# Optimization experiments

Hardware: AMD Instinct MI355X
Metric: run time of the kernel (lower is better)

## Reference

```python
import jax, jax.numpy as jnp
import numpy as np

LATENT = 512
RNN = 512
CODE = 512
INP = 2
MIX = 5
BATCH = 4096
SEGMENTS = 512


def _p(key, shape, scale=0.05):
    return jax.random.normal(key, shape, dtype=jnp.float32) * scale


def setup_inputs() -> dict:
    key = jax.random.key(0)
    ks = jax.random.split(key, 20)
    return {
        "latent": jax.random.normal(ks[0], (BATCH, LATENT), dtype=jnp.float32),
        "W_unpack": _p(ks[1], (CODE, LATENT)),
        "b_unpack": _p(ks[2], (CODE,)),
        "W_ih1": _p(ks[3], (4 * RNN, CODE + INP)),
        "W_hh1": _p(ks[4], (4 * RNN, RNN)),
        "b_ih1": _p(ks[5], (4 * RNN,)),
        "b_hh1": _p(ks[6], (4 * RNN,)),
        "W_ih2": _p(ks[7], (4 * RNN, RNN)),
        "W_hh2": _p(ks[8], (4 * RNN, RNN)),
        "b_ih2": _p(ks[9], (4 * RNN,)),
        "b_hh2": _p(ks[10], (4 * RNN,)),
        "W_mu": _p(ks[11], (MIX, RNN)),
        "b_mu": _p(ks[12], (MIX,)),
        "W_var": _p(ks[13], (MIX, RNN)),
        "b_var": _p(ks[14], (MIX,)),
        "W_mix": _p(ks[15], (MIX, RNN)),
        "b_mix": _p(ks[16], (MIX,)),
        "eps": jax.random.normal(ks[17], (SEGMENTS, BATCH, 1), dtype=jnp.float32),
        "num_segments": SEGMENTS,
    }


def _lstm_cell(x, h, c, W_ih, W_hh, b_ih, b_hh):
    # PyTorch LSTMCell: gate order i, f, g, o
    gates = x @ W_ih.T + b_ih + h @ W_hh.T + b_hh
    i, f, g, o = jnp.split(gates, 4, axis=-1)
    c_new = jax.nn.sigmoid(f) * c + jax.nn.sigmoid(i) * jnp.tanh(g)
    h_new = jax.nn.sigmoid(o) * jnp.tanh(c_new)
    return h_new, c_new


def reference(latent, W_unpack, b_unpack, W_ih1, W_hh1, b_ih1, b_hh1,
              W_ih2, W_hh2, b_ih2, b_hh2, W_mu, b_mu, W_var, b_var,
              W_mix, b_mix, eps, num_segments):
    t = 0.0  # default temperature arg
    B = latent.shape[0]
    idea = jnp.tanh(latent @ W_unpack.T + b_unpack)  # [B, CODE]

    def step(carry, eps_s):
        prev, h1, c1, h2, c2 = carry
        x = jnp.concatenate([idea, prev], axis=-1)          # [B, CODE+2]
        h1, c1 = _lstm_cell(x, h1, c1, W_ih1, W_hh1, b_ih1, b_hh1)
        h2, c2 = _lstm_cell(h1, h2, c2, W_ih2, W_hh2, b_ih2, b_hh2)
        rho = jax.nn.softmax(h2 @ W_mix.T + b_mix, axis=-1)  # [B, MIX]
        mu = jnp.sum(rho * (h2 @ W_mu.T + b_mu), axis=-1, keepdims=True)
        sigma = jnp.sum(rho * jnp.exp(h2 @ W_var.T + b_var - t), axis=-1, keepdims=True)
        angles = jnp.tanh(mu + sigma * eps_s)                # rsample + tanh, [B, 1]
        prev = jnp.concatenate([angles, jnp.zeros_like(angles)], axis=-1)
        return (prev, h1, c1, h2, c2), angles

    z = jnp.zeros((B, RNN), dtype=latent.dtype)
    carry0 = (jnp.zeros((B, INP), dtype=latent.dtype), z, z, z, z)
    _, angles = jax.lax.scan(step, carry0, eps)              # [S, B, 1]
    level = jnp.concatenate([angles, jnp.zeros_like(angles)], axis=-1)  # [S, B, 2]
    return jnp.transpose(level, (1, 0, 2))                   # [B, S, 2]
```

## Files before the change

kernel.cpp:

```cpp
#include <hip/hip_runtime.h>
#include <stdint.h>

#define BATCH 4096
#define RNN   512
#define SEGS  512

typedef __attribute__((ext_vector_type(8))) short bf16x8;
typedef __attribute__((ext_vector_type(4))) float f32x4;

#define MODE_TANH  0
#define MODE_BASE  1
#define MODE_CELL1 2
#define MODE_CELL2 3

__device__ __forceinline__ unsigned short f2bf(float f){
  unsigned u = __float_as_uint(f);
  u += 0x7FFF + ((u >> 16) & 1);
  return (unsigned short)(u >> 16);
}
__device__ __forceinline__ float bf2f(unsigned short s){
  return __uint_as_float(((unsigned)s) << 16);
}
__device__ __forceinline__ float fsigmoid(float x){ return 1.0f / (1.0f + __expf(-x)); }
__device__ __forceinline__ float ftanh(float x){
  float e = __expf(-2.0f * fabsf(x));
  float t = (1.0f - e) / (1.0f + e);
  return copysignf(t, x);
}


__global__ void prep_cvt(const float* __restrict__ x, short* __restrict__ y, int n){
  int i = blockIdx.x * 256 + threadIdx.x;
  if (i < n) y[i] = (short)f2bf(x[i]);
}

__global__ void prep_reorder(
    const float* __restrict__ W_ih1, const float* __restrict__ W_hh1,
    const float* __restrict__ b_ih1, const float* __restrict__ b_hh1,
    const float* __restrict__ W_ih2, const float* __restrict__ W_hh2,
    const float* __restrict__ b_ih2, const float* __restrict__ b_hh2,
    short* __restrict__ Wr1, short* __restrict__ W1c,
    short* __restrict__ Wr2i, short* __restrict__ Wr2h,
    float* __restrict__ w1r, float* __restrict__ b1r, float* __restrict__ b2r)
{
  int idx = blockIdx.x * 256 + threadIdx.x;
  if (idx >= 2048 * 512) return;
  int rn = idx >> 9;
  int k  = idx & 511;
  int j = rn >> 2, g = rn & 3;
  int ro = g * 512 + j;
  Wr1 [idx] = (short)f2bf(W_hh1[(size_t)ro * 512 + k]);
  W1c [idx] = (short)f2bf(W_ih1[(size_t)ro * 514 + k]);
  Wr2i[idx] = (short)f2bf(W_ih2[(size_t)ro * 512 + k]);
  Wr2h[idx] = (short)f2bf(W_hh2[(size_t)ro * 512 + k]);
  if (k == 0){
    w1r[rn] = W_ih1[(size_t)ro * 514 + 512];
    b1r[rn] = b_ih1[ro] + b_hh1[ro];
    b2r[rn] = b_ih2[ro] + b_hh2[ro];
  }
}

__global__ __launch_bounds__(256) void gemm_fused(
    const short* __restrict__ A1, const short* __restrict__ B1,
    const short* __restrict__ A2, const short* __restrict__ B2,
    int k1, int k2, int N, int mode,
    const float* __restrict__ bias,
    const float* __restrict__ base1,
    const float* __restrict__ w1r,
    const float* __restrict__ ang,
    float* __restrict__ cbuf,
    void* __restrict__ outp)
{
  __shared__ __align__(16) short As[128 * 72];
  __shared__ __align__(16) short Bs[128 * 72];
  const int tid  = threadIdx.x;
  const int lane = tid & 63;
  const int wave = tid >> 6;
  const int wm = wave >> 1, wn = wave & 1;
  const int m0 = blockIdx.y * 128, n0 = blockIdx.x * 128;

  f32x4 acc[4][4];
  #pragma unroll
  for (int i = 0; i < 4; i++)
    #pragma unroll
    for (int j = 0; j < 4; j++)
      acc[i][j] = (f32x4){0.f, 0.f, 0.f, 0.f};

  const int nk = (k1 + k2) >> 6;
  for (int it = 0; it < nk; ++it){
    int ko = it << 6;
    const short* Ap; const short* Bp; int kk;
    if (ko < k1){ Ap = A1; Bp = B1; kk = ko; }
    else        { Ap = A2; Bp = B2; kk = ko - k1; }
    #pragma unroll
    for (int i = 0; i < 4; i++){
      int c = i * 256 + tid;
      int row = c >> 3, c8 = (c & 7) << 3;
      *(uint4*)&As[row * 72 + c8] = *(const uint4*)&Ap[(size_t)(m0 + row) * 512 + kk + c8];
      *(uint4*)&Bs[row * 72 + c8] = *(const uint4*)&Bp[(size_t)(n0 + row) * 512 + kk + c8];
    }
    __syncthreads();
    #pragma unroll
    for (int kw = 0; kw < 2; ++kw){
      bf16x8 af[4], bfr[4];
      const int ro = (lane & 15) * 72 + kw * 32 + (lane >> 4) * 8;
      #pragma unroll
      for (int f = 0; f < 4; f++){
        af[f]  = *(const bf16x8*)&As[(wm * 64 + f * 16) * 72 + ro];
        bfr[f] = *(const bf16x8*)&Bs[(wn * 64 + f * 16) * 72 + ro];
      }
      #pragma unroll
      for (int mf = 0; mf < 4; mf++)
        #pragma unroll
        for (int nf = 0; nf < 4; nf++)
          acc[mf][nf] = __builtin_amdgcn_mfma_f32_16x16x32_bf16(af[mf], bfr[nf], acc[mf][nf], 0, 0, 0);
    }
    __syncthreads();
  }

  const int lr = (lane >> 4) * 4;
  const int lc = lane & 15;

  if (mode == MODE_TANH){
    unsigned short* out = (unsigned short*)outp;
    #pragma unroll
    for (int mf = 0; mf < 4; mf++)
      #pragma unroll
      for (int nf = 0; nf < 4; nf++)
        #pragma unroll
        for (int r = 0; r < 4; r++){
          int grow = m0 + wm * 64 + mf * 16 + lr + r;
          int gcol = n0 + wn * 64 + nf * 16 + lc;
          float v = acc[mf][nf][r] + bias[gcol];
          out[(size_t)grow * N + gcol] = f2bf(ftanh(v));
        }
  } else if (mode == MODE_BASE){
    float* out = (float*)outp;
    #pragma unroll
    for (int mf = 0; mf < 4; mf++)
      #pragma unroll
      for (int nf = 0; nf < 4; nf++)
        #pragma unroll
        for (int r = 0; r < 4; r++){
          int grow = m0 + wm * 64 + mf * 16 + lr + r;
          int gcol = n0 + wn * 64 + nf * 16 + lc;
          out[(size_t)grow * N + gcol] = acc[mf][nf][r] + bias[gcol];
        }
  } else {
    unsigned short* hout = (unsigned short*)outp;
    const int q = lane & 3;
    #pragma unroll
    for (int mf = 0; mf < 4; mf++)
      #pragma unroll
      for (int nf = 0; nf < 4; nf++)
        #pragma unroll
        for (int r = 0; r < 4; r++){
          int grow = m0 + wm * 64 + mf * 16 + lr + r;
          int gcol = n0 + wn * 64 + nf * 16 + lc;
          float v = acc[mf][nf][r];
          if (mode == MODE_CELL1)
            v += base1[(size_t)grow * 2048 + gcol] + ang[grow] * w1r[gcol];
          else
            v += bias[gcol];
          float x1 = __shfl_xor(v, 1);
          float x2 = __shfl_xor(v, 2);
          float x3 = __shfl_xor(v, 3);
          if (q == 0){
            int j = gcol >> 2;
            size_t ci = (size_t)grow * 512 + j;
            float co = cbuf[ci];
            float cn = fsigmoid(x1) * co + fsigmoid(v) * ftanh(x2);
            float hn = fsigmoid(x3) * ftanh(cn);
            cbuf[ci] = cn;
            hout[ci] = f2bf(hn);
          }
        }
  }
}

__global__ __launch_bounds__(256) void head_step(
    const short* __restrict__ h2,
    const float* __restrict__ Wmu,  const float* __restrict__ bmu,
    const float* __restrict__ Wvar, const float* __restrict__ bvar,
    const float* __restrict__ Wmix, const float* __restrict__ bmix,
    const float* __restrict__ eps,  float* __restrict__ ang,
    float* __restrict__ out, int s)
{
  const int lane = threadIdx.x & 63;
  const int wave = threadIdx.x >> 6;
  const int row = blockIdx.x * 4 + wave;

  uint4 hv = *(const uint4*)&h2[(size_t)row * 512 + lane * 8];
  const unsigned short* hs = (const unsigned short*)&hv;
  float h[8];
  #pragma unroll
  for (int j = 0; j < 8; j++) h[j] = bf2f(hs[j]);

  float p[15];
  #pragma unroll
  for (int k = 0; k < 5; k++){
    const float4* wm4 = (const float4*)(Wmu  + (size_t)k * 512 + lane * 8);
    const float4* wv4 = (const float4*)(Wvar + (size_t)k * 512 + lane * 8);
    const float4* wx4 = (const float4*)(Wmix + (size_t)k * 512 + lane * 8);
    float4 a0 = wm4[0], a1 = wm4[1];
    float4 v0 = wv4[0], v1 = wv4[1];
    float4 x0 = wx4[0], x1 = wx4[1];
    p[k]      = h[0]*a0.x + h[1]*a0.y + h[2]*a0.z + h[3]*a0.w + h[4]*a1.x + h[5]*a1.y + h[6]*a1.z + h[7]*a1.w;
    p[5 + k]  = h[0]*v0.x + h[1]*v0.y + h[2]*v0.z + h[3]*v0.w + h[4]*v1.x + h[5]*v1.y + h[6]*v1.z + h[7]*v1.w;
    p[10 + k] = h[0]*x0.x + h[1]*x0.y + h[2]*x0.z + h[3]*x0.w + h[4]*x1.x + h[5]*x1.y + h[6]*x1.z + h[7]*x1.w;
  }
  #pragma unroll
  for (int k = 0; k < 15; k++){
    #pragma unroll
    for (int off = 1; off < 64; off <<= 1)
      p[k] += __shfl_xor(p[k], off);
  }
  if (lane == 0){
    float l[5], mx = -1e30f;
    #pragma unroll
    for (int k = 0; k < 5; k++){ l[k] = p[10 + k] + bmix[k]; mx = fmaxf(mx, l[k]); }
    float se = 0.f, e[5];
    #pragma unroll
    for (int k = 0; k < 5; k++){ e[k] = __expf(l[k] - mx); se += e[k]; }
    float inv = 1.0f / se, mu = 0.f, sg = 0.f;
    #pragma unroll
    for (int k = 0; k < 5; k++){
      float rho = e[k] * inv;
      mu += rho * (p[k] + bmu[k]);
      sg += rho * __expf(p[5 + k] + bvar[k]);
    }
    float a = ftanh(mu + sg * eps[(size_t)s * BATCH + row]);
    ang[row] = a;
    size_t o = ((size_t)row * SEGS + s) * 2;
    out[o]     = a;
    out[o + 1] = 0.0f;
  }
}


extern "C" void kernel_launch(void* const* d_in, const int* in_sizes, int n_in,
                              void* d_out, int out_size, void* d_ws, size_t ws_size,
                              hipStream_t stream)
{
  const float* latent   = (const float*)d_in[0];
  const float* W_unpack = (const float*)d_in[1];
  const float* b_unpack = (const float*)d_in[2];
  const float* W_ih1    = (const float*)d_in[3];
  const float* W_hh1    = (const float*)d_in[4];
  const float* b_ih1    = (const float*)d_in[5];
  const float* b_hh1    = (const float*)d_in[6];
  const float* W_ih2    = (const float*)d_in[7];
  const float* W_hh2    = (const float*)d_in[8];
  const float* b_ih2    = (const float*)d_in[9];
  const float* b_hh2    = (const float*)d_in[10];
  const float* W_mu     = (const float*)d_in[11];
  const float* b_mu     = (const float*)d_in[12];
  const float* W_var    = (const float*)d_in[13];
  const float* b_var    = (const float*)d_in[14];
  const float* W_mix    = (const float*)d_in[15];
  const float* b_mix    = (const float*)d_in[16];
  const float* eps      = (const float*)d_in[17];
  float* out = (float*)d_out;

  char* p = (char*)d_ws;
  auto alloc = [&](size_t b) -> void* {
    void* r = (void*)p;
    p += (b + 255) & ~(size_t)255;
    return r;
  };
  short* latb  = (short*)alloc((size_t)BATCH * 512 * 2);
  short* Wub   = (short*)alloc((size_t)512 * 512 * 2);
  short* idea  = (short*)alloc((size_t)BATCH * 512 * 2);
  float* base1 = (float*)alloc((size_t)BATCH * 2048 * 4);
  short* Wr1   = (short*)alloc((size_t)2048 * 512 * 2);
  short* W1c   = (short*)alloc((size_t)2048 * 512 * 2);
  short* Wr2i  = (short*)alloc((size_t)2048 * 512 * 2);
  short* Wr2h  = (short*)alloc((size_t)2048 * 512 * 2);
  float* w1r   = (float*)alloc(2048 * 4);
  float* b1r   = (float*)alloc(2048 * 4);
  float* b2r   = (float*)alloc(2048 * 4);
  short* h1a   = (short*)alloc((size_t)BATCH * 512 * 2);
  short* h1b   = (short*)alloc((size_t)BATCH * 512 * 2);
  short* h2a   = (short*)alloc((size_t)BATCH * 512 * 2);
  short* h2b   = (short*)alloc((size_t)BATCH * 512 * 2);
  float* c1    = (float*)alloc((size_t)BATCH * 512 * 4);
  float* c2    = (float*)alloc((size_t)BATCH * 512 * 4);
  float* ang   = (float*)alloc(BATCH * 4);
  short* h1[2] = {h1a, h1b};
  short* h2[2] = {h2a, h2b};

  hipMemsetAsync(h1[0], 0, (size_t)BATCH * 512 * 2, stream);
  hipMemsetAsync(h2[0], 0, (size_t)BATCH * 512 * 2, stream);
  hipMemsetAsync(c1, 0, (size_t)BATCH * 512 * 4, stream);
  hipMemsetAsync(c2, 0, (size_t)BATCH * 512 * 4, stream);
  hipMemsetAsync(ang, 0, BATCH * 4, stream);

  prep_cvt<<<(BATCH * 512) / 256, 256, 0, stream>>>(latent, latb, BATCH * 512);
  prep_cvt<<<(512 * 512) / 256, 256, 0, stream>>>(W_unpack, Wub, 512 * 512);
  prep_reorder<<<(2048 * 512) / 256, 256, 0, stream>>>(
      W_ih1, W_hh1, b_ih1, b_hh1, W_ih2, W_hh2, b_ih2, b_hh2,
      Wr1, W1c, Wr2i, Wr2h, w1r, b1r, b2r);

  dim3 blk(256);
  gemm_fused<<<dim3(512 / 128, 32), blk, 0, stream>>>(
      latb, Wub, nullptr, nullptr, 512, 0, 512, MODE_TANH,
      b_unpack, nullptr, nullptr, nullptr, nullptr, (void*)idea);
  gemm_fused<<<dim3(2048 / 128, 32), blk, 0, stream>>>(
      idea, W1c, nullptr, nullptr, 512, 0, 2048, MODE_BASE,
      b1r, nullptr, nullptr, nullptr, nullptr, (void*)base1);

  int cur = 0;
  for (int s = 0; s < SEGS; ++s){
    gemm_fused<<<dim3(16, 32), blk, 0, stream>>>(
        h1[cur], Wr1, nullptr, nullptr, 512, 0, 2048, MODE_CELL1,
        nullptr, base1, w1r, ang, c1, (void*)h1[cur ^ 1]);
    gemm_fused<<<dim3(16, 32), blk, 0, stream>>>(
        h1[cur ^ 1], Wr2i, h2[cur], Wr2h, 512, 512, 2048, MODE_CELL2,
        b2r, nullptr, nullptr, nullptr, c2, (void*)h2[cur ^ 1]);
    head_step<<<BATCH / 4, 256, 0, stream>>>(
        h2[cur ^ 1], W_mu, b_mu, W_var, b_var, W_mix, b_mix, eps, ang, out, s);
    cur ^= 1;
  }
}
```

Baseline: 63.81 ms.

## Replace per-step kernel launches with a persistent RNN kernel using group barriers

Replaces the 1536 per-step launches (two LSTM GEMMs plus head) with one persistent kernel of 256 blocks. Each block owns a 128x256 tile, and blocks covering the same 128 rows synchronise through atomic counters in global memory. The rewrite also loads tiles with direct global-to-LDS loads in a swizzled layout, stores base1 in bf16 with a row-interleaved layout, and folds the mixture head into the kernel with bf16 weights. This removes launch overhead and inter-kernel gaps, but relies on all 256 blocks being co-resident to avoid deadlock and adds spin-wait costs.

Measured after the change: 202.8 ms. +217.8%, slower.

```diff
diff --git a/kernel.cpp b/kernel.cpp
--- a/kernel.cpp
+++ b/kernel.cpp
@@ -2,16 +2,14 @@
 #include <stdint.h>
 
 #define BATCH 4096
-#define RNN   512
 #define SEGS  512
 
 typedef __attribute__((ext_vector_type(8))) short bf16x8;
 typedef __attribute__((ext_vector_type(4))) float f32x4;
 
-#define MODE_TANH  0
-#define MODE_BASE  1
-#define MODE_CELL1 2
-#define MODE_CELL2 3
+#define GLD_LDS16(g, l) \
+  __builtin_amdgcn_global_load_lds((const __attribute__((address_space(1))) void*)(g), \
+                                   (__attribute__((address_space(3))) void*)(l), 16, 0, 0)
 
 __device__ __forceinline__ unsigned short f2bf(float f){
   unsigned u = __float_as_uint(f);
@@ -60,25 +58,38 @@
   }
 }
 
-__global__ __launch_bounds__(256) void gemm_fused(
-    const short* __restrict__ A1, const short* __restrict__ B1,
-    const short* __restrict__ A2, const short* __restrict__ B2,
-    int k1, int k2, int N, int mode,
-    const float* __restrict__ bias,
-    const float* __restrict__ base1,
-    const float* __restrict__ w1r,
-    const float* __restrict__ ang,
-    float* __restrict__ cbuf,
-    void* __restrict__ outp)
+__global__ void prep_whead(const float* __restrict__ Wmu, const float* __restrict__ Wvar,
+                           const float* __restrict__ Wmix, short* __restrict__ Wh){
+  int i = blockIdx.x * 256 + threadIdx.x;
+  if (i >= 15 * 512) return;
+  int n = i >> 9, k = i & 511;
+  float v = (n < 5) ? Wmu[n * 512 + k] : (n < 10) ? Wvar[(n - 5) * 512 + k]
+          : Wmix[(n - 10) * 512 + k];
+  Wh[i] = (short)f2bf(v);
+}
+
+__global__ __launch_bounds__(256) void gemm_pre(
+    const short* A, const short* B,
+    int N, int mode, const float* bias,
+    unsigned short* outp)
 {
-  __shared__ __align__(16) short As[128 * 72];
-  __shared__ __align__(16) short Bs[128 * 72];
-  const int tid  = threadIdx.x;
-  const int lane = tid & 63;
-  const int wave = tid >> 6;
+  __shared__ __align__(16) short As[8192];
+  __shared__ __align__(16) short Bs[8192];
+  const int tid = threadIdx.x, lane = tid & 63, wave = tid >> 6;
   const int wm = wave >> 1, wn = wave & 1;
   const int m0 = blockIdx.y * 128, n0 = blockIdx.x * 128;
 
+  int aoff[4], boff[4];
+  #pragma unroll
+  for (int j = 0; j < 4; j++){
+    int c = (wave * 4 + j) * 64 + lane;
+    int quad = c & 3, r16 = (c >> 2) & 15, kw = (c >> 6) & 1, g = c >> 7;
+    int row = g * 16 + r16, col = kw * 32 + quad * 8;
+    aoff[j] = (m0 + row) * 512 + col;
+    boff[j] = (n0 + row) * 512 + col;
+  }
+  const int fro = ((lane & 15) * 4 + (lane >> 4)) * 8;
+
   f32x4 acc[4][4];
   #pragma unroll
   for (int i = 0; i < 4; i++)
@@ -86,28 +97,21 @@
     for (int j = 0; j < 4; j++)
       acc[i][j] = (f32x4){0.f, 0.f, 0.f, 0.f};
 
-  const int nk = (k1 + k2) >> 6;
-  for (int it = 0; it < nk; ++it){
-    int ko = it << 6;
-    const short* Ap; const short* Bp; int kk;
-    if (ko < k1){ Ap = A1; Bp = B1; kk = ko; }
-    else        { Ap = A2; Bp = B2; kk = ko - k1; }
-    #pragma unroll
-    for (int i = 0; i < 4; i++){
-      int c = i * 256 + tid;
-      int row = c >> 3, c8 = (c & 7) << 3;
-      *(uint4*)&As[row * 72 + c8] = *(const uint4*)&Ap[(size_t)(m0 + row) * 512 + kk + c8];
-      *(uint4*)&Bs[row * 72 + c8] = *(const uint4*)&Bp[(size_t)(n0 + row) * 512 + kk + c8];
+  for (int it = 0; it < 8; ++it){
+    const int kk = it << 6;
+    #pragma unroll
+    for (int j = 0; j < 4; ++j){
+      GLD_LDS16(A + aoff[j] + kk, (char*)As + (wave * 4 + j) * 1024);
+      GLD_LDS16(B + boff[j] + kk, (char*)Bs + (wave * 4 + j) * 1024);
     }
     __syncthreads();
     #pragma unroll
     for (int kw = 0; kw < 2; ++kw){
       bf16x8 af[4], bfr[4];
-      const int ro = (lane & 15) * 72 + kw * 32 + (lane >> 4) * 8;
       #pragma unroll
       for (int f = 0; f < 4; f++){
-        af[f]  = *(const bf16x8*)&As[(wm * 64 + f * 16) * 72 + ro];
-        bfr[f] = *(const bf16x8*)&Bs[(wn * 64 + f * 16) * 72 + ro];
+        af[f]  = *(const bf16x8*)&As[((wm * 4 + f) * 2 + kw) * 512 + fro];
+        bfr[f] = *(const bf16x8*)&Bs[((wn * 4 + f) * 2 + kw) * 512 + fro];
       }
       #pragma unroll
       for (int mf = 0; mf < 4; mf++)
@@ -120,120 +124,260 @@
 
   const int lr = (lane >> 4) * 4;
   const int lc = lane & 15;
-
-  if (mode == MODE_TANH){
-    unsigned short* out = (unsigned short*)outp;
-    #pragma unroll
-    for (int mf = 0; mf < 4; mf++)
-      #pragma unroll
-      for (int nf = 0; nf < 4; nf++)
-        #pragma unroll
-        for (int r = 0; r < 4; r++){
-          int grow = m0 + wm * 64 + mf * 16 + lr + r;
-          int gcol = n0 + wn * 64 + nf * 16 + lc;
-          float v = acc[mf][nf][r] + bias[gcol];
-          out[(size_t)grow * N + gcol] = f2bf(ftanh(v));
-        }
-  } else if (mode == MODE_BASE){
-    float* out = (float*)outp;
-    #pragma unroll
-    for (int mf = 0; mf < 4; mf++)
-      #pragma unroll
-      for (int nf = 0; nf < 4; nf++)
-        #pragma unroll
-        for (int r = 0; r < 4; r++){
-          int grow = m0 + wm * 64 + mf * 16 + lr + r;
-          int gcol = n0 + wn * 64 + nf * 16 + lc;
-          out[(size_t)grow * N + gcol] = acc[mf][nf][r] + bias[gcol];
-        }
-  } else {
-    unsigned short* hout = (unsigned short*)outp;
-    const int q = lane & 3;
-    #pragma unroll
-    for (int mf = 0; mf < 4; mf++)
-      #pragma unroll
-      for (int nf = 0; nf < 4; nf++)
-        #pragma unroll
-        for (int r = 0; r < 4; r++){
-          int grow = m0 + wm * 64 + mf * 16 + lr + r;
-          int gcol = n0 + wn * 64 + nf * 16 + lc;
-          float v = acc[mf][nf][r];
-          if (mode == MODE_CELL1)
-            v += base1[(size_t)grow * 2048 + gcol] + ang[grow] * w1r[gcol];
-          else
-            v += bias[gcol];
-          float x1 = __shfl_xor(v, 1);
-          float x2 = __shfl_xor(v, 2);
-          float x3 = __shfl_xor(v, 3);
-          if (q == 0){
-            int j = gcol >> 2;
-            size_t ci = (size_t)grow * 512 + j;
-            float co = cbuf[ci];
-            float cn = fsigmoid(x1) * co + fsigmoid(v) * ftanh(x2);
-            float hn = fsigmoid(x3) * ftanh(cn);
-            cbuf[ci] = cn;
-            hout[ci] = f2bf(hn);
+  #pragma unroll
+  for (int mf = 0; mf < 4; mf++)
+    #pragma unroll
+    for (int nf = 0; nf < 4; nf++)
+      #pragma unroll
+      for (int r = 0; r < 4; r++){
+        int grow = m0 + wm * 64 + mf * 16 + lr + r;
+        int gcol = n0 + wn * 64 + nf * 16 + lc;
+        float v = acc[mf][nf][r] + bias[gcol];
+        if (mode == 0)
+          outp[(size_t)grow * N + gcol] = f2bf(ftanh(v));
+        else
+          outp[((size_t)(grow >> 2) * 2048 + gcol) * 4 + (grow & 3)] = f2bf(v);
+      }
+}
+
+
+__device__ __forceinline__ void run_tile256(
+    const short* A1, const short* B1, const short* A2, const short* B2,
+    int nk1, int nk2, const int* aoff, const int* boff,
+    short* As, short* Bs, int wave, int wm, int wn, int fro,
+    f32x4 (&acc)[4][8])
+{
+  #pragma unroll
+  for (int i = 0; i < 4; i++)
+    #pragma unroll
+    for (int j = 0; j < 8; j++)
+      acc[i][j] = (f32x4){0.f, 0.f, 0.f, 0.f};
+
+  const int nk = nk1 + nk2;
+  for (int it = 0; it < nk; ++it){
+    const short* Ap = (it < nk1) ? A1 : A2;
+    const short* Bp = (it < nk1) ? B1 : B2;
+    const int kk = ((it < nk1) ? it : it - nk1) << 6;
+    #pragma unroll
+    for (int j = 0; j < 4; ++j)
+      GLD_LDS16(Ap + aoff[j] + kk, (char*)As + (wave * 4 + j) * 1024);
+    #pragma unroll
+    for (int j = 0; j < 8; ++j)
+      GLD_LDS16(Bp + boff[j] + kk, (char*)Bs + (wave * 8 + j) * 1024);
+    __syncthreads();
+    #pragma unroll
+    for (int kw = 0; kw < 2; ++kw){
+      bf16x8 af[4], bfr[8];
+      #pragma unroll
+      for (int f = 0; f < 4; f++)
+        af[f]  = *(const bf16x8*)&As[((wm * 4 + f) * 2 + kw) * 512 + fro];
+      #pragma unroll
+      for (int f = 0; f < 8; f++)
+        bfr[f] = *(const bf16x8*)&Bs[((wn * 8 + f) * 2 + kw) * 512 + fro];
+      #pragma unroll
+      for (int mf = 0; mf < 4; mf++)
+        #pragma unroll
+        for (int nf = 0; nf < 8; nf++)
+          acc[mf][nf] = __builtin_amdgcn_mfma_f32_16x16x32_bf16(af[mf], bfr[nf], acc[mf][nf], 0, 0, 0);
+    }
+    __syncthreads();
+  }
+}
+
+__device__ __forceinline__ void mgroup_bar(int* cnt, int target, int tid){
+  __syncthreads();
+  if (tid == 0){
+    __threadfence();
+    __hip_atomic_fetch_add(cnt, 1, __ATOMIC_RELEASE, __HIP_MEMORY_SCOPE_AGENT);
+    while (__hip_atomic_load(cnt, __ATOMIC_ACQUIRE, __HIP_MEMORY_SCOPE_AGENT) < target)
+      __builtin_amdgcn_s_sleep(1);
+    __threadfence();
+  }
+  __syncthreads();
+}
+
+__global__ __launch_bounds__(256, 1) void persistent_rnn(
+    short* h1A, short* h1B, short* h2A, short* h2B,
+    const short* Wr1, const short* Wr2i, const short* Wr2h,
+    const unsigned short* base1,
+    const float* w1r, const float* b2r,
+    const short* Whead,
+    const float* bmu, const float* bvar,
+    const float* bmix, const float* eps,
+    float* angG, float* c1G, float* c2G,
+    int* barA, int* barB, int* flagH,
+    float* out)
+{
+  __shared__ __align__(16) short As[8192];
+  __shared__ __align__(16) short Bs[16384];
+  __shared__ float headP[16 * 16];
+  __shared__ float angSf[128];
+
+  const int tid = threadIdx.x, lane = tid & 63, wave = tid >> 6;
+  const int wm = wave >> 1, wn = wave & 1;
+  const int bid = blockIdx.x;
+  const int m_idx = bid >> 3, n_idx = bid & 7;
+  const int m0 = m_idx * 128, n0 = n_idx * 256;
+
+  int aoff[4], boff[8];
+  #pragma unroll
+  for (int j = 0; j < 4; j++){
+    int c = (wave * 4 + j) * 64 + lane;
+    int quad = c & 3, r16 = (c >> 2) & 15, kw = (c >> 6) & 1, g = c >> 7;
+    aoff[j] = (m0 + g * 16 + r16) * 512 + kw * 32 + quad * 8;
+  }
+  #pragma unroll
+  for (int j = 0; j < 8; j++){
+    int c = (wave * 8 + j) * 64 + lane;
+    int quad = c & 3, r16 = (c >> 2) & 15, kw = (c >> 6) & 1, g = c >> 7;
+    boff[j] = (n0 + g * 16 + r16) * 512 + kw * 32 + quad * 8;
+  }
+  const int fro = ((lane & 15) * 4 + (lane >> 4)) * 8;
+  const int lr = (lane >> 4) * 4;
+  const int lc = lane & 15;
+  const int q = lane & 3;
+
+  if (tid < 128) angSf[tid] = 0.f;
+  __syncthreads();
+
+  f32x4 acc[4][8];
+  short* h1buf[2] = {h1A, h1B};
+  short* h2buf[2] = {h2A, h2B};
+  int cur = 0;
+
+  #pragma clang loop unroll(disable)
+  for (int s = 0; s < SEGS; ++s){
+    const short* h1c = h1buf[cur];
+    short*       h1n = h1buf[cur ^ 1];
+    const short* h2c = h2buf[cur];
+    short*       h2n = h2buf[cur ^ 1];
+
+    run_tile256(h1c, Wr1, nullptr, nullptr, 8, 0, aoff, boff,
+                As, Bs, wave, wm, wn, fro, acc);
+
+    if (s > 0){
+      if (tid == 0){
+        while (__hip_atomic_load(&flagH[m_idx], __ATOMIC_ACQUIRE, __HIP_MEMORY_SCOPE_AGENT) < 8 * s)
+          __builtin_amdgcn_s_sleep(1);
+        __threadfence();
+      }
+      __syncthreads();
+      if (tid < 128)
+        angSf[tid] = __hip_atomic_load(&angG[m0 + tid], __ATOMIC_RELAXED, __HIP_MEMORY_SCOPE_AGENT);
+      __syncthreads();
+    }
+
+    {
+      unsigned short* hout = (unsigned short*)h1n;
+      #pragma unroll
+      for (int mf = 0; mf < 4; mf++)
+        #pragma unroll
+        for (int nf = 0; nf < 8; nf++){
+          const int growb = m0 + wm * 64 + mf * 16 + lr;
+          const int gcol  = n0 + wn * 128 + nf * 16 + lc;
+          const float wv = w1r[gcol];
+          ushort4 b4 = *(const ushort4*)&base1[((size_t)(growb >> 2) * 2048 + gcol) * 4];
+          const unsigned short bb4[4] = {b4.x, b4.y, b4.z, b4.w};
+          #pragma unroll
+          for (int r = 0; r < 4; r++){
+            int grow = growb + r;
+            float v = acc[mf][nf][r] + bf2f(bb4[r]) + angSf[grow - m0] * wv;
+            float x1 = __shfl_xor(v, 1);
+            float x2 = __shfl_xor(v, 2);
+            float x3 = __shfl_xor(v, 3);
+            if (q == 0){
+              size_t ci = (size_t)grow * 512 + (gcol >> 2);
+              float co = c1G[ci];
+              float cn = fsigmoid(x1) * co + fsigmoid(v) * ftanh(x2);
+              float hn = fsigmoid(x3) * ftanh(cn);
+              c1G[ci] = cn;
+              hout[ci] = f2bf(hn);
+            }
           }
         }
-  }
-}
-
-__global__ __launch_bounds__(256) void head_step(
-    const short* __restrict__ h2,
-    const float* __restrict__ Wmu,  const float* __restrict__ bmu,
-    const float* __restrict__ Wvar, const float* __restrict__ bvar,
-    const float* __restrict__ Wmix, const float* __restrict__ bmix,
-    const float* __restrict__ eps,  float* __restrict__ ang,
-    float* __restrict__ out, int s)
-{
-  const int lane = threadIdx.x & 63;
-  const int wave = threadIdx.x >> 6;
-  const int row = blockIdx.x * 4 + wave;
-
-  uint4 hv = *(const uint4*)&h2[(size_t)row * 512 + lane * 8];
-  const unsigned short* hs = (const unsigned short*)&hv;
-  float h[8];
-  #pragma unroll
-  for (int j = 0; j < 8; j++) h[j] = bf2f(hs[j]);
-
-  float p[15];
-  #pragma unroll
-  for (int k = 0; k < 5; k++){
-    const float4* wm4 = (const float4*)(Wmu  + (size_t)k * 512 + lane * 8);
-    const float4* wv4 = (const float4*)(Wvar + (size_t)k * 512 + lane * 8);
-    const float4* wx4 = (const float4*)(Wmix + (size_t)k * 512 + lane * 8);
-    float4 a0 = wm4[0], a1 = wm4[1];
-    float4 v0 = wv4[0], v1 = wv4[1];
-    float4 x0 = wx4[0], x1 = wx4[1];
-    p[k]      = h[0]*a0.x + h[1]*a0.y + h[2]*a0.z + h[3]*a0.w + h[4]*a1.x + h[5]*a1.y + h[6]*a1.z + h[7]*a1.w;
-    p[5 + k]  = h[0]*v0.x + h[1]*v0.y + h[2]*v0.z + h[3]*v0.w + h[4]*v1.x + h[5]*v1.y + h[6]*v1.z + h[7]*v1.w;
-    p[10 + k] = h[0]*x0.x + h[1]*x0.y + h[2]*x0.z + h[3]*x0.w + h[4]*x1.x + h[5]*x1.y + h[6]*x1.z + h[7]*x1.w;
-  }
-  #pragma unroll
-  for (int k = 0; k < 15; k++){
-    #pragma unroll
-    for (int off = 1; off < 64; off <<= 1)
-      p[k] += __shfl_xor(p[k], off);
-  }
-  if (lane == 0){
-    float l[5], mx = -1e30f;
-    #pragma unroll
-    for (int k = 0; k < 5; k++){ l[k] = p[10 + k] + bmix[k]; mx = fmaxf(mx, l[k]); }
-    float se = 0.f, e[5];
-    #pragma unroll
-    for (int k = 0; k < 5; k++){ e[k] = __expf(l[k] - mx); se += e[k]; }
-    float inv = 1.0f / se, mu = 0.f, sg = 0.f;
-    #pragma unroll
-    for (int k = 0; k < 5; k++){
-      float rho = e[k] * inv;
-      mu += rho * (p[k] + bmu[k]);
-      sg += rho * __expf(p[5 + k] + bvar[k]);
-    }
-    float a = ftanh(mu + sg * eps[(size_t)s * BATCH + row]);
-    ang[row] = a;
-    size_t o = ((size_t)row * SEGS + s) * 2;
-    out[o]     = a;
-    out[o + 1] = 0.0f;
+    }
+    mgroup_bar(&barA[m_idx], 8 * (s + 1), tid);
+
+    run_tile256(h1n, Wr2i, h2c, Wr2h, 8, 8, aoff, boff,
+                As, Bs, wave, wm, wn, fro, acc);
+    {
+      unsigned short* hout = (unsigned short*)h2n;
+      #pragma unroll
+      for (int mf = 0; mf < 4; mf++)
+        #pragma unroll
+        for (int nf = 0; nf < 8; nf++){
+          const int growb = m0 + wm * 64 + mf * 16 + lr;
+          const int gcol  = n0 + wn * 128 + nf * 16 + lc;
+          const float bv = b2r[gcol];
+          #pragma unroll
+          for (int r = 0; r < 4; r++){
+            int grow = growb + r;
+            float v = acc[mf][nf][r] + bv;
+            float x1 = __shfl_xor(v, 1);
+            float x2 = __shfl_xor(v, 2);
+            float x3 = __shfl_xor(v, 3);
+            if (q == 0){
+              size_t ci = (size_t)grow * 512 + (gcol >> 2);
+              float co = c2G[ci];
+              float cn = fsigmoid(x1) * co + fsigmoid(v) * ftanh(x2);
+              float hn = fsigmoid(x3) * ftanh(cn);
+              c2G[ci] = cn;
+              hout[ci] = f2bf(hn);
+            }
+          }
+        }
+    }
+    mgroup_bar(&barB[m_idx], 8 * (s + 1), tid);
+
+    {
+      const int rr = tid & 15, o = tid >> 4;
+      const int row = m0 + n_idx * 16 + rr;
+      if (o < 15){
+        float pv = 0.f;
+        const unsigned short* hp = (const unsigned short*)h2n + (size_t)row * 512;
+        const unsigned short* wp = (const unsigned short*)Whead + o * 512;
+        for (int k = 0; k < 64; k++){
+          uint4 hv = *(const uint4*)(hp + k * 8);
+          uint4 wv = *(const uint4*)(wp + k * 8);
+          const unsigned short* hh = (const unsigned short*)&hv;
+          const unsigned short* ww = (const unsigned short*)&wv;
+          #pragma unroll
+          for (int e = 0; e < 8; e++)
+            pv += bf2f(hh[e]) * bf2f(ww[e]);
+        }
+        headP[rr * 16 + o] = pv;
+      }
+      __syncthreads();
+      if (tid < 16){
+        float pp[15];
+        #pragma unroll
+        for (int k = 0; k < 15; k++) pp[k] = headP[tid * 16 + k];
+        float l[5], mx = -1e30f;
+        #pragma unroll
+        for (int k = 0; k < 5; k++){ l[k] = pp[10 + k] + bmix[k]; mx = fmaxf(mx, l[k]); }
+        float se = 0.f, e5[5];
+        #pragma unroll
+        for (int k = 0; k < 5; k++){ e5[k] = __expf(l[k] - mx); se += e5[k]; }
+        float inv = 1.0f / se, mu = 0.f, sg = 0.f;
+        #pragma unroll
+        for (int k = 0; k < 5; k++){
+          float rho = e5[k] * inv;
+          mu += rho * (pp[k] + bmu[k]);
+          sg += rho * __expf(pp[5 + k] + bvar[k]);
+        }
+        const int row2 = m0 + n_idx * 16 + tid;
+        float a = ftanh(mu + sg * eps[(size_t)s * BATCH + row2]);
+        __hip_atomic_store(&angG[row2], a, __ATOMIC_RELAXED, __HIP_MEMORY_SCOPE_AGENT);
+        size_t oo = ((size_t)row2 * SEGS + s) * 2;
+        out[oo] = a; out[oo + 1] = 0.0f;
+      }
+      __syncthreads();
+      if (tid == 0){
+        __threadfence();
+        __hip_atomic_fetch_add(&flagH[m_idx], 1, __ATOMIC_RELEASE, __HIP_MEMORY_SCOPE_AGENT);
+      }
+    }
+    cur ^= 1;
   }
 }
 
@@ -271,11 +415,12 @@
   short* latb  = (short*)alloc((size_t)BATCH * 512 * 2);
   short* Wub   = (short*)alloc((size_t)512 * 512 * 2);
   short* idea  = (short*)alloc((size_t)BATCH * 512 * 2);
-  float* base1 = (float*)alloc((size_t)BATCH * 2048 * 4);
+  unsigned short* base1 = (unsigned short*)alloc((size_t)BATCH * 2048 * 2);
   short* Wr1   = (short*)alloc((size_t)2048 * 512 * 2);
   short* W1c   = (short*)alloc((size_t)2048 * 512 * 2);
   short* Wr2i  = (short*)alloc((size_t)2048 * 512 * 2);
   short* Wr2h  = (short*)alloc((size_t)2048 * 512 * 2);
+  short* Whead = (short*)alloc((size_t)15 * 512 * 2);
   float* w1r   = (float*)alloc(2048 * 4);
   float* b1r   = (float*)alloc(2048 * 4);
   float* b2r   = (float*)alloc(2048 * 4);
@@ -286,39 +431,30 @@
   float* c1    = (float*)alloc((size_t)BATCH * 512 * 4);
   float* c2    = (float*)alloc((size_t)BATCH * 512 * 4);
   float* ang   = (float*)alloc(BATCH * 4);
-  short* h1[2] = {h1a, h1b};
-  short* h2[2] = {h2a, h2b};
-
-  hipMemsetAsync(h1[0], 0, (size_t)BATCH * 512 * 2, stream);
-  hipMemsetAsync(h2[0], 0, (size_t)BATCH * 512 * 2, stream);
-  hipMemsetAsync(c1, 0, (size_t)BATCH * 512 * 4, stream);
-  hipMemsetAsync(c2, 0, (size_t)BATCH * 512 * 4, stream);
-  hipMemsetAsync(ang, 0, BATCH * 4, stream);
+  int*   barA  = (int*)alloc(32 * 4);
+  int*   barB  = (int*)alloc(32 * 4);
+  int*   flagH = (int*)alloc(32 * 4);
+
+  (void)hipMemsetAsync(h1a, 0, (size_t)BATCH * 512 * 2, stream);
+  (void)hipMemsetAsync(h2a, 0, (size_t)BATCH * 512 * 2, stream);
+  (void)hipMemsetAsync(c1, 0, (size_t)BATCH * 512 * 4, stream);
+  (void)hipMemsetAsync(c2, 0, (size_t)BATCH * 512 * 4, stream);
+  (void)hipMemsetAsync(barA, 0, 32 * 4, stream);
+  (void)hipMemsetAsync(barB, 0, 32 * 4, stream);
+  (void)hipMemsetAsync(flagH, 0, 32 * 4, stream);
 
   prep_cvt<<<(BATCH * 512) / 256, 256, 0, stream>>>(latent, latb, BATCH * 512);
   prep_cvt<<<(512 * 512) / 256, 256, 0, stream>>>(W_unpack, Wub, 512 * 512);
   prep_reorder<<<(2048 * 512) / 256, 256, 0, stream>>>(
       W_ih1, W_hh1, b_ih1, b_hh1, W_ih2, W_hh2, b_ih2, b_hh2,
       Wr1, W1c, Wr2i, Wr2h, w1r, b1r, b2r);
-
-  dim3 blk(256);
-  gemm_fused<<<dim3(512 / 128, 32), blk, 0, stream>>>(
-      latb, Wub, nullptr, nullptr, 512, 0, 512, MODE_TANH,
-      b_unpack, nullptr, nullptr, nullptr, nullptr, (void*)idea);
-  gemm_fused<<<dim3(2048 / 128, 32), blk, 0, stream>>>(
-      idea, W1c, nullptr, nullptr, 512, 0, 2048, MODE_BASE,
-      b1r, nullptr, nullptr, nullptr, nullptr, (void*)base1);
-
-  int cur = 0;
-  for (int s = 0; s < SEGS; ++s){
-    gemm_fused<<<dim3(16, 32), blk, 0, stream>>>(
-        h1[cur], Wr1, nullptr, nullptr, 512, 0, 2048, MODE_CELL1,
-        nullptr, base1, w1r, ang, c1, (void*)h1[cur ^ 1]);
-    gemm_fused<<<dim3(16, 32), blk, 0, stream>>>(
-        h1[cur ^ 1], Wr2i, h2[cur], Wr2h, 512, 512, 2048, MODE_CELL2,
-        b2r, nullptr, nullptr, nullptr, c2, (void*)h2[cur ^ 1]);
-    head_step<<<BATCH / 4, 256, 0, stream>>>(
-        h2[cur ^ 1], W_mu, b_mu, W_var, b_var, W_mix, b_mix, eps, ang, out, s);
-    cur ^= 1;
-  }
-}
+  prep_whead<<<30, 256, 0, stream>>>(W_mu, W_var, W_mix, Whead);
+
+  gemm_pre<<<dim3(4, 32), 256, 0, stream>>>(latb, Wub, 512, 0, b_unpack,
+                                            (unsigned short*)idea);
+  gemm_pre<<<dim3(16, 32), 256, 0, stream>>>(idea, W1c, 2048, 1, b1r, base1);
+
+  persistent_rnn<<<256, 256, 0, stream>>>(
+      h1a, h1b, h2a, h2b, Wr1, Wr2i, Wr2h, base1, w1r, b2r,
+      Whead, b_mu, b_var, b_mix, eps, ang, c1, c2, barA, barB, flagH, out);
+}
```
